# Kernel tuning notes

Hardware: AMD Instinct MI355X
Metric: run time of the kernel (lower is better)

Reference implementation:

```python
import jax, jax.numpy as jnp
import numpy as np

N = 50000       # nodes
E = 1600000     # edges
IN_C = 128
HID = 32        # hidden_channels per head
HEADS = 4
OUT_C = 64
SLOPE = 0.2     # PyG GATConv default negative_slope


def setup_inputs() -> dict:
    key = jax.random.key(0)
    ks = jax.random.split(key, 10)
    s1 = 1.0 / np.sqrt(IN_C)
    s2 = 1.0 / np.sqrt(HEADS * HID)
    return {
        "x": jax.random.normal(ks[0], (N, IN_C), dtype=jnp.float32),
        "edge_index": jax.random.randint(ks[1], (2, E), 0, N, dtype=jnp.int64),
        "W1": jax.random.normal(ks[2], (IN_C, HEADS * HID), dtype=jnp.float32) * s1,
        "a1_src": jax.random.normal(ks[3], (HEADS, HID), dtype=jnp.float32) * s2,
        "a1_dst": jax.random.normal(ks[4], (HEADS, HID), dtype=jnp.float32) * s2,
        "b1": jnp.zeros((HEADS * HID,), dtype=jnp.float32),
        "W2": jax.random.normal(ks[5], (HEADS * HID, OUT_C), dtype=jnp.float32) * s2,
        "a2_src": jax.random.normal(ks[6], (1, OUT_C), dtype=jnp.float32) * (1.0 / np.sqrt(OUT_C)),
        "a2_dst": jax.random.normal(ks[7], (1, OUT_C), dtype=jnp.float32) * (1.0 / np.sqrt(OUT_C)),
        "b2": jnp.zeros((OUT_C,), dtype=jnp.float32),
    }


def gat_conv(x, W, a_src, a_dst, b, src, dst, n, heads, out_c, concat):
    # Linear projection per head: [n, heads, out_c]
    h = (x @ W).reshape(n, heads, out_c)
    # Per-node attention halves (PyG decomposition of a^T [h_i || h_j])
    al_src = jnp.sum(h * a_src, axis=-1)  # [n, heads]
    al_dst = jnp.sum(h * a_dst, axis=-1)  # [n, heads]
    # Per-edge logits + segment softmax over destination nodes
    e = jax.nn.leaky_relu(al_src[src] + al_dst[dst], SLOPE)  # [e, heads]
    m = jax.ops.segment_max(e, dst, num_segments=n)          # [n, heads]
    ex = jnp.exp(e - m[dst])
    denom = jax.ops.segment_sum(ex, dst, num_segments=n)
    alpha = ex / denom[dst]                                   # [e, heads]
    # Weighted scatter-aggregate of source features
    out = jax.ops.segment_sum(h[src] * alpha[..., None], dst, num_segments=n)
    out = out.reshape(n, heads * out_c) if concat else out.mean(axis=1)
    return out + b


def reference(x, edge_index, W1, a1_src, a1_dst, b1, W2, a2_src, a2_dst, b2):
    # PyG GATConv adds self-loops by default
    loops = jnp.arange(N, dtype=edge_index.dtype)
    src = jnp.concatenate([edge_index[0], loops])
    dst = jnp.concatenate([edge_index[1], loops])
    h = jax.nn.elu(gat_conv(x, W1, a1_src, a1_dst, b1, src, dst, N, HEADS, HID, True))
    out = gat_conv(h, W2, a2_src, a2_dst, b2, src, dst, N, 1, OUT_C, True)
    return out
```

## Files before the change

kernel.cpp:

```cpp
#include <hip/hip_runtime.h>
#include <hip/hip_fp16.h>

#define LRELU(v) ((v) > 0.f ? (v) : 0.2f * (v))

typedef _Float16 f16;
typedef __attribute__((ext_vector_type(4))) _Float16 f16x4;
typedef __attribute__((ext_vector_type(8))) _Float16 f16x8;
typedef __attribute__((ext_vector_type(4))) float    f32x4;

__device__ __forceinline__ int swz(int row, int kbyte) {
    return (row * 256 + kbyte) ^ ((row & 7) << 4);
}

constexpr int NPB    = 128;
constexpr int MAXBUK = 512;
constexpr int EPB    = 8192;
constexpr int CAP    = 12288;

__global__ void zero_kernel(int* __restrict__ p, int n) {
    int i = blockIdx.x * blockDim.x + threadIdx.x;
    if (i < n) p[i] = 0;
}

__global__ __launch_bounds__(256) void bucket_hist_kernel(
    const int* __restrict__ ei, int* __restrict__ bcnt, int E, int tot, int nbuk) {
    __shared__ int lh[MAXBUK];
    for (int i = threadIdx.x; i < nbuk; i += 256) lh[i] = 0;
    __syncthreads();
    int base = blockIdx.x * EPB;
    int lim  = min(base + EPB, tot);
    for (int e = base + threadIdx.x; e < lim; e += 256) {
        int dst = (e < E) ? ei[E + e] : (e - E);
        atomicAdd(&lh[dst >> 7], 1);
    }
    __syncthreads();
    for (int i = threadIdx.x; i < nbuk; i += 256)
        if (lh[i]) atomicAdd(&bcnt[i], lh[i]);
}

__global__ __launch_bounds__(512) void bucket_scan_kernel(
    const int* __restrict__ bcnt, int* __restrict__ boff, int* __restrict__ bcur,
    int* __restrict__ csr_off, int nbuk, int n, int tot) {
    __shared__ int s[512];
    int t = threadIdx.x;
    int v0 = (t < nbuk) ? bcnt[t] : 0;
    s[t] = v0;
    __syncthreads();
    for (int d = 1; d < 512; d <<= 1) {
        int v = (t >= d) ? s[t - d] : 0;
        __syncthreads();
        s[t] += v;
        __syncthreads();
    }
    if (t < nbuk) {
        int off = s[t] - v0;
        boff[t] = off;
        bcur[t] = off;
    }
    if (t == 0) { boff[nbuk] = tot; csr_off[n] = tot; }
}

__global__ __launch_bounds__(256) void bucket_scatter_kernel(
    const int* __restrict__ ei, int* __restrict__ bcur, int2* __restrict__ be,
    int E, int tot, int nbuk) {
    __shared__ int lh[MAXBUK];
    __shared__ int lb[MAXBUK];
    for (int i = threadIdx.x; i < nbuk; i += 256) lh[i] = 0;
    __syncthreads();
    int base = blockIdx.x * EPB;
    int lim  = min(base + EPB, tot);
    for (int e = base + threadIdx.x; e < lim; e += 256) {
        int dst = (e < E) ? ei[E + e] : (e - E);
        atomicAdd(&lh[dst >> 7], 1);
    }
    __syncthreads();
    for (int i = threadIdx.x; i < nbuk; i += 256)
        lb[i] = lh[i] ? atomicAdd(&bcur[i], lh[i]) : 0;
    __syncthreads();
    for (int i = threadIdx.x; i < nbuk; i += 256) lh[i] = 0;
    __syncthreads();
    for (int e = base + threadIdx.x; e < lim; e += 256) {
        int src, dst;
        if (e < E) { src = ei[e]; dst = ei[E + e]; }
        else       { src = dst = e - E; }
        int b = dst >> 7;
        int p = lb[b] + atomicAdd(&lh[b], 1);
        be[p] = make_int2(src, dst);
    }
}

__global__ __launch_bounds__(256) void csr_build_kernel(
    const int2* __restrict__ be, const int* __restrict__ boff,
    int* __restrict__ csr_off, int* __restrict__ csr_src, int n) {
    __shared__ int hist[NPB];
    __shared__ int sc[NPB];
    __shared__ int cur[NPB];
    __shared__ int stage[CAP];
    const int b = blockIdx.x, t = threadIdx.x;
    const int start = boff[b], end = boff[b + 1], cnt = end - start;
    if (t < NPB) hist[t] = 0;
    __syncthreads();
    for (int i = t; i < cnt; i += 256)
        atomicAdd(&hist[be[start + i].y & (NPB - 1)], 1);
    __syncthreads();
    if (t < NPB) sc[t] = hist[t];
    __syncthreads();
    for (int d = 1; d < NPB; d <<= 1) {
        int v = (t < NPB && t >= d) ? sc[t - d] : 0;
        __syncthreads();
        if (t < NPB) sc[t] += v;
        __syncthreads();
    }
    if (t < NPB) {
        int excl = sc[t] - hist[t];
        cur[t] = excl;
        int node = b * NPB + t;
        if (node < n) csr_off[node] = start + excl;
    }
    __syncthreads();
    if (cnt <= CAP) {
        for (int i = t; i < cnt; i += 256) {
            int2 e = be[start + i];
            int  p = atomicAdd(&cur[e.y & (NPB - 1)], 1);
            stage[p] = e.x;
        }
        __syncthreads();
        for (int i = t; i < cnt; i += 256) csr_src[start + i] = stage[i];
    } else {
        for (int i = t; i < cnt; i += 256) {
            int2 e = be[start + i];
            int  p = atomicAdd(&cur[e.y & (NPB - 1)], 1);
            csr_src[start + p] = e.x;
        }
    }
}

__global__ void hist_kernel(const int* __restrict__ ei, int* __restrict__ counts,
                            int E, int tot) {
    int e = blockIdx.x * blockDim.x + threadIdx.x;
    if (e >= tot) return;
    int dst = (e < E) ? ei[E + e] : (e - E);
    atomicAdd(&counts[dst], 1);
}

__global__ __launch_bounds__(1024) void scan_kernel(const int* __restrict__ counts,
                                                    int* __restrict__ csr_off,
                                                    int* __restrict__ cursor, int n) {
    __shared__ int part[1024];
    int t = threadIdx.x;
    int chunk = (n + 1023) >> 10;
    int lo = t * chunk, hi = min(lo + chunk, n);
    int sum = 0;
    for (int i = lo; i < hi; ++i) sum += counts[i];
    part[t] = sum;
    __syncthreads();
    for (int d = 1; d < 1024; d <<= 1) {
        int add = (t >= d) ? part[t - d] : 0;
        __syncthreads();
        part[t] += add;
        __syncthreads();
    }
    int run = part[t] - sum;
    for (int i = lo; i < hi; ++i) {
        csr_off[i] = run;
        cursor[i]  = run;
        run += counts[i];
    }
    if (t == 1023) csr_off[n] = part[1023];
}

__global__ void scatter_kernel(const int* __restrict__ ei, int* __restrict__ cursor,
                               int* __restrict__ csr_src, int E, int tot) {
    int e = blockIdx.x * blockDim.x + threadIdx.x;
    if (e >= tot) return;
    int src, dst;
    if (e < E) { src = ei[e]; dst = ei[E + e]; }
    else       { src = dst = e - E; }
    int pos = atomicAdd(&cursor[dst], 1);
    csr_src[pos] = src;
}

__global__ void prep_w_kernel(const float* __restrict__ W, f16* __restrict__ WhT,
                              f16* __restrict__ WlT, int ncol) {
    int idx = blockIdx.x * 256 + threadIdx.x;
    if (idx >= 128 * ncol) return;
    int k = idx / ncol, c = idx % ncol;
    float v = W[idx];
    f16 h = (f16)v;
    f16 l = (f16)(v - (float)h);
    int byte = swz(c, k * 2);
    *(f16*)((char*)WhT + byte) = h;
    *(f16*)((char*)WlT + byte) = l;
}

template <int NCOL>
__global__ __launch_bounds__(256) void gemm_mfma_kernel(
    const float* __restrict__ x, const f16* __restrict__ WhT,
    const f16* __restrict__ WlT, __half* __restrict__ feat, int n) {
    constexpr int ROWS = 64;
    constexpr int NCT  = NCOL / 16;
    __shared__ char Xh[ROWS * 256];
    __shared__ char Xl[ROWS * 256];
    __shared__ char Wh[NCOL * 256];
    __shared__ char Wl[NCOL * 256];
    const int t  = threadIdx.x;
    const int r0 = blockIdx.x * ROWS;

    {
        const float4* sh = (const float4*)WhT;
        const float4* sl = (const float4*)WlT;
        float4* dh = (float4*)Wh;
        float4* dl = (float4*)Wl;
        for (int i = t; i < NCOL * 16; i += 256) { dh[i] = sh[i]; dl[i] = sl[i]; }
    }
    {
        const float4* X4 = (const float4*)x;
        for (int i = t; i < ROWS * 32; i += 256) {
            int row = i >> 5, k4 = i & 31;
            float4 v = (r0 + row < n) ? X4[(size_t)(r0 + row) * 32 + k4]
                                      : make_float4(0.f, 0.f, 0.f, 0.f);
            f16x4 h, l;
            h[0] = (f16)v.x; l[0] = (f16)(v.x - (float)h[0]);
            h[1] = (f16)v.y; l[1] = (f16)(v.y - (float)h[1]);
            h[2] = (f16)v.z; l[2] = (f16)(v.z - (float)h[2]);
            h[3] = (f16)v.w; l[3] = (f16)(v.w - (float)h[3]);
            int byte = swz(row, k4 * 8);
            *(f16x4*)(Xh + byte) = h;
            *(f16x4*)(Xl + byte) = l;
        }
    }
    __syncthreads();

    const int w  = t >> 6, l = t & 63;
    const int lr = l & 15, lg = l >> 4;
    const int arow = w * 16 + lr;

    f32x4 acc[NCT];
#pragma unroll
    for (int ct = 0; ct < NCT; ++ct) acc[ct] = (f32x4){0.f, 0.f, 0.f, 0.f};

#pragma unroll
    for (int kt = 0; kt < 4; ++kt) {
        const int ka = kt * 64 + 8 * lg;
        f16x4 al0 = *(const f16x4*)(Xh + swz(arow, ka));
        f16x4 al1 = *(const f16x4*)(Xh + swz(arow, ka + 32));
        f16x4 am0 = *(const f16x4*)(Xl + swz(arow, ka));
        f16x4 am1 = *(const f16x4*)(Xl + swz(arow, ka + 32));
        f16x8 a_h = __builtin_shufflevector(al0, al1, 0, 1, 2, 3, 4, 5, 6, 7);
        f16x8 a_l = __builtin_shufflevector(am0, am1, 0, 1, 2, 3, 4, 5, 6, 7);
#pragma unroll
        for (int ct = 0; ct < NCT; ++ct) {
            const int col = ct * 16 + lr;
            f16x4 b0 = *(const f16x4*)(Wh + swz(col, ka));
            f16x4 b1 = *(const f16x4*)(Wh + swz(col, ka + 32));
            f16x4 c0 = *(const f16x4*)(Wl + swz(col, ka));
            f16x4 c1 = *(const f16x4*)(Wl + swz(col, ka + 32));
            f16x8 b_h = __builtin_shufflevector(b0, b1, 0, 1, 2, 3, 4, 5, 6, 7);
            f16x8 b_l = __builtin_shufflevector(c0, c1, 0, 1, 2, 3, 4, 5, 6, 7);
            acc[ct] = __builtin_amdgcn_mfma_f32_16x16x32_f16(a_h, b_h, acc[ct], 0, 0, 0);
            acc[ct] = __builtin_amdgcn_mfma_f32_16x16x32_f16(a_l, b_h, acc[ct], 0, 0, 0);
            acc[ct] = __builtin_amdgcn_mfma_f32_16x16x32_f16(a_h, b_l, acc[ct], 0, 0, 0);
        }
    }

#pragma unroll
    for (int ct = 0; ct < NCT; ++ct)
#pragma unroll
        for (int r = 0; r < 4; ++r) {
            int grow = r0 + w * 16 + lg * 4 + r;
            if (grow < n)
                feat[(size_t)grow * NCOL + ct * 16 + lr] = __float2half(acc[ct][r]);
        }
}

template <int OUTC, int HEADS>
__global__ __launch_bounds__(256) void al_kernel(
    const __half* __restrict__ feat, const float* __restrict__ a_src,
    const float* __restrict__ a_dst, float* __restrict__ alsrc,
    float* __restrict__ aldst, int n) {
    constexpr int CP  = OUTC / 64;
    constexpr int HID = OUTC / HEADS;
    constexpr int G   = HID / CP;
    int node = blockIdx.x * 4 + (threadIdx.x >> 6);
    int lane = threadIdx.x & 63;
    if (node >= n) return;
    float s, d;
    if constexpr (CP == 2) {
        __half2 hv = *(const __half2*)(feat + (size_t)node * OUTC + lane * 2);
        float2  f  = __half22float2(hv);
        s = f.x * a_src[lane * 2] + f.y * a_src[lane * 2 + 1];
        d = f.x * a_dst[lane * 2] + f.y * a_dst[lane * 2 + 1];
    } else {
        float f = __half2float(feat[(size_t)node * OUTC + lane]);
        s = f * a_src[lane];
        d = f * a_dst[lane];
    }
#pragma unroll
    for (int o = G / 2; o > 0; o >>= 1) {
        s += __shfl_xor(s, o);
        d += __shfl_xor(d, o);
    }
    if ((lane & (G - 1)) == 0) {
        int h = lane / G;
        alsrc[node * HEADS + h] = s;
        aldst[node * HEADS + h] = d;
    }
}

template <int OUTC, int HEADS, bool DO_ELU>
__global__ __launch_bounds__(256) void aggregate_kernel(
    const int* __restrict__ csr_off, const int* __restrict__ csr_src,
    const float* __restrict__ alsrc, const float* __restrict__ aldst,
    const __half* __restrict__ feat, const float* __restrict__ bias,
    float* __restrict__ out, int n) {
    constexpr int CPL = 8;
    constexpr int LPE = OUTC / CPL;
    constexpr int EPW = 64 / LPE;
    constexpr int HID = OUTC / HEADS;
    int node = blockIdx.x * 4 + (threadIdx.x >> 6);
    int lane = threadIdx.x & 63;
    if (node >= n) return;
    int off = csr_off[node];
    int deg = csr_off[node + 1] - off;

    const int   sub = lane / LPE;
    const int   l   = lane % LPE;
    const int   h   = (CPL * l) / HID;
    const float ad  = aldst[node * HEADS + h];

    float acc[CPL];
#pragma unroll
    for (int c = 0; c < CPL; ++c) acc[c] = 0.f;
    float sume = 0.f;

#pragma unroll 2
    for (int i = sub; i < deg; i += EPW) {
        int   s = csr_src[off + i];
        float e = alsrc[(size_t)s * HEADS + h] + ad;
        e = LRELU(e);
        float p = __expf(e);
        sume += p;
        const float4   fv = *(const float4*)(feat + (size_t)s * OUTC + CPL * l);
        const __half2* hp = (const __half2*)&fv;
#pragma unroll
        for (int c2 = 0; c2 < 4; ++c2) {
            float2 f2 = __half22float2(hp[c2]);
            acc[2 * c2 + 0] += p * f2.x;
            acc[2 * c2 + 1] += p * f2.y;
        }
    }
#pragma unroll
    for (int o = LPE; o < 64; o <<= 1) {
#pragma unroll
        for (int c = 0; c < CPL; ++c) acc[c] += __shfl_xor(acc[c], o);
        sume += __shfl_xor(sume, o);
    }
    if (sub == 0) {
        const float inv = 1.f / sume;
        float v[CPL];
#pragma unroll
        for (int c = 0; c < CPL; ++c) {
            v[c] = acc[c] * inv + bias[CPL * l + c];
            if (DO_ELU) v[c] = (v[c] > 0.f) ? v[c] : expm1f(v[c]);
        }
        float* op = out + (size_t)node * OUTC + CPL * l;
        *(float4*)(op + 0) = make_float4(v[0], v[1], v[2], v[3]);
        *(float4*)(op + 4) = make_float4(v[4], v[5], v[6], v[7]);
    }
}

extern "C" void kernel_launch(void* const* d_in, const int* in_sizes, int n_in,
                              void* d_out, int out_size, void* d_ws, size_t ws_size,
                              hipStream_t stream) {
    const float* x   = (const float*)d_in[0];
    const int*   ei  = (const int*)d_in[1];
    const float* W1  = (const float*)d_in[2];
    const float* a1s = (const float*)d_in[3];
    const float* a1d = (const float*)d_in[4];
    const float* b1  = (const float*)d_in[5];
    const float* W2  = (const float*)d_in[6];
    const float* a2s = (const float*)d_in[7];
    const float* a2d = (const float*)d_in[8];
    const float* b2  = (const float*)d_in[9];
    float*       out = (float*)d_out;

    constexpr int IN_C = 128, HEADS = 4, OUTC1 = 128, OUTC2 = 64;
    const int n    = in_sizes[0] / IN_C;
    const int E    = in_sizes[1] / 2;
    const int tot  = E + n;
    const int nbuk = (n + NPB - 1) / NPB;

    char* w = (char*)d_ws;
    auto  alloc = [&](size_t bytes) -> char* {
        char* p = w;
        w += (bytes + 255) & ~(size_t)255;
        return p;
    };
    int*    bcnt    = (int*)alloc((size_t)MAXBUK * 4);
    int*    boff    = (int*)alloc((size_t)(MAXBUK + 1) * 4);
    int*    bcur    = (int*)alloc((size_t)MAXBUK * 4);
    int*    csr_off = (int*)alloc((size_t)(n + 1) * 4);
    int*    csr_src = (int*)alloc((size_t)tot * 4);
    int2*   be      = (int2*)alloc((size_t)tot * 8);
    size_t  csr_need = (size_t)(w - (char*)d_ws);
    f16*    wh1     = (f16*)alloc(128 * 256);
    f16*    wl1     = (f16*)alloc(128 * 256);
    f16*    wh2     = (f16*)alloc(64 * 256);
    f16*    wl2     = (f16*)alloc(64 * 256);
    float*  alsrc1  = (float*)alloc((size_t)n * HEADS * 4);
    float*  aldst1  = (float*)alloc((size_t)n * HEADS * 4);
    float*  alsrc2  = (float*)alloc((size_t)n * 4);
    float*  aldst2  = (float*)alloc((size_t)n * 4);
    __half* feat_h  = (__half*)alloc((size_t)n * OUTC1 * 2);
    float*  y1      = (float*)alloc((size_t)n * OUTC1 * 4);
    const bool new_csr = (nbuk <= MAXBUK) && (csr_need <= ws_size);

    prep_w_kernel<<<(128 * OUTC1 + 255) / 256, 256, 0, stream>>>(W1, wh1, wl1, OUTC1);
    prep_w_kernel<<<(128 * OUTC2 + 255) / 256, 256, 0, stream>>>(W2, wh2, wl2, OUTC2);

    if (new_csr) {
        const int g1 = (tot + EPB - 1) / EPB;
        zero_kernel<<<(nbuk + 255) / 256, 256, 0, stream>>>(bcnt, nbuk);
        bucket_hist_kernel<<<g1, 256, 0, stream>>>(ei, bcnt, E, tot, nbuk);
        bucket_scan_kernel<<<1, 512, 0, stream>>>(bcnt, boff, bcur, csr_off, nbuk, n, tot);
        bucket_scatter_kernel<<<g1, 256, 0, stream>>>(ei, bcur, be, E, tot, nbuk);
        csr_build_kernel<<<nbuk, 256, 0, stream>>>(be, boff, csr_off, csr_src, n);
    } else {
        int* counts = (int*)be;
        int* cursor = counts + n;
        zero_kernel<<<(n + 255) / 256, 256, 0, stream>>>(counts, n);
        hist_kernel<<<(tot + 255) / 256, 256, 0, stream>>>(ei, counts, E, tot);
        scan_kernel<<<1, 1024, 0, stream>>>(counts, csr_off, cursor, n);
        scatter_kernel<<<(tot + 255) / 256, 256, 0, stream>>>(ei, cursor, csr_src, E, tot);
    }

    const int gblk = (n + 63) / 64;
    gemm_mfma_kernel<OUTC1><<<gblk, 256, 0, stream>>>(x, wh1, wl1, feat_h, n);
    al_kernel<OUTC1, HEADS><<<(n + 3) / 4, 256, 0, stream>>>(
        feat_h, a1s, a1d, alsrc1, aldst1, n);
    aggregate_kernel<OUTC1, HEADS, true><<<(n + 3) / 4, 256, 0, stream>>>(
        csr_off, csr_src, alsrc1, aldst1, feat_h, b1, y1, n);

    gemm_mfma_kernel<OUTC2><<<gblk, 256, 0, stream>>>(y1, wh2, wl2, feat_h, n);
    al_kernel<OUTC2, 1><<<(n + 3) / 4, 256, 0, stream>>>(
        feat_h, a2s, a2d, alsrc2, aldst2, n);
    aggregate_kernel<OUTC2, 1, false><<<(n + 3) / 4, 256, 0, stream>>>(
        csr_off, csr_src, alsrc2, aldst2, feat_h, b2, out, n);
}
```

Measured before the change: 222.6 us.

## Fuse attention-logit computation into GEMM, pack bucket edges, batch softmax weights

```diff
diff --git a/kernel.cpp b/kernel.cpp
--- a/kernel.cpp
+++ b/kernel.cpp
@@ -14,7 +14,7 @@
 
 constexpr int NPB    = 128;
 constexpr int MAXBUK = 512;
-constexpr int EPB    = 8192;
+constexpr int EPB    = 2048;
 constexpr int CAP    = 12288;
 
 __global__ void zero_kernel(int* __restrict__ p, int n) {
@@ -61,8 +61,8 @@
 }
 
 __global__ __launch_bounds__(256) void bucket_scatter_kernel(
-    const int* __restrict__ ei, int* __restrict__ bcur, int2* __restrict__ be,
-    int E, int tot, int nbuk) {
+    const int* __restrict__ ei, int* __restrict__ bcur,
+    unsigned int* __restrict__ be, int E, int tot, int nbuk) {
     __shared__ int lh[MAXBUK];
     __shared__ int lb[MAXBUK];
     for (int i = threadIdx.x; i < nbuk; i += 256) lh[i] = 0;
@@ -85,12 +85,12 @@
         else       { src = dst = e - E; }
         int b = dst >> 7;
         int p = lb[b] + atomicAdd(&lh[b], 1);
-        be[p] = make_int2(src, dst);
+        be[p] = (unsigned)src | ((unsigned)(dst & (NPB - 1)) << 16);
     }
 }
 
 __global__ __launch_bounds__(256) void csr_build_kernel(
-    const int2* __restrict__ be, const int* __restrict__ boff,
+    const unsigned int* __restrict__ be, const int* __restrict__ boff,
     int* __restrict__ csr_off, int* __restrict__ csr_src, int n) {
     __shared__ int hist[NPB];
     __shared__ int sc[NPB];
@@ -101,7 +101,7 @@
     if (t < NPB) hist[t] = 0;
     __syncthreads();
     for (int i = t; i < cnt; i += 256)
-        atomicAdd(&hist[be[start + i].y & (NPB - 1)], 1);
+        atomicAdd(&hist[be[start + i] >> 16], 1);
     __syncthreads();
     if (t < NPB) sc[t] = hist[t];
     __syncthreads();
@@ -120,17 +120,17 @@
     __syncthreads();
     if (cnt <= CAP) {
         for (int i = t; i < cnt; i += 256) {
-            int2 e = be[start + i];
-            int  p = atomicAdd(&cur[e.y & (NPB - 1)], 1);
-            stage[p] = e.x;
+            unsigned v = be[start + i];
+            int p = atomicAdd(&cur[v >> 16], 1);
+            stage[p] = (int)(v & 0xFFFFu);
         }
         __syncthreads();
         for (int i = t; i < cnt; i += 256) csr_src[start + i] = stage[i];
     } else {
         for (int i = t; i < cnt; i += 256) {
-            int2 e = be[start + i];
-            int  p = atomicAdd(&cur[e.y & (NPB - 1)], 1);
-            csr_src[start + p] = e.x;
+            unsigned v = be[start + i];
+            int p = atomicAdd(&cur[v >> 16], 1);
+            csr_src[start + p] = (int)(v & 0xFFFFu);
         }
     }
 }
@@ -193,12 +193,15 @@
     *(f16*)((char*)WlT + byte) = l;
 }
 
-template <int NCOL>
+template <int NCOL, int HEADS>
 __global__ __launch_bounds__(256) void gemm_mfma_kernel(
     const float* __restrict__ x, const f16* __restrict__ WhT,
-    const f16* __restrict__ WlT, __half* __restrict__ feat, int n) {
+    const f16* __restrict__ WlT, const float* __restrict__ a_src,
+    const float* __restrict__ a_dst, __half* __restrict__ feat,
+    float* __restrict__ alsrc, float* __restrict__ aldst, int n) {
     constexpr int ROWS = 64;
     constexpr int NCT  = NCOL / 16;
+    constexpr int CTH  = (NCOL / HEADS) / 16;
     __shared__ char Xh[ROWS * 256];
     __shared__ char Xl[ROWS * 256];
     __shared__ char Wh[NCOL * 256];
@@ -271,39 +274,35 @@
             if (grow < n)
                 feat[(size_t)grow * NCOL + ct * 16 + lr] = __float2half(acc[ct][r]);
         }
-}
-
-template <int OUTC, int HEADS>
-__global__ __launch_bounds__(256) void al_kernel(
-    const __half* __restrict__ feat, const float* __restrict__ a_src,
-    const float* __restrict__ a_dst, float* __restrict__ alsrc,
-    float* __restrict__ aldst, int n) {
-    constexpr int CP  = OUTC / 64;
-    constexpr int HID = OUTC / HEADS;
-    constexpr int G   = HID / CP;
-    int node = blockIdx.x * 4 + (threadIdx.x >> 6);
-    int lane = threadIdx.x & 63;
-    if (node >= n) return;
-    float s, d;
-    if constexpr (CP == 2) {
-        __half2 hv = *(const __half2*)(feat + (size_t)node * OUTC + lane * 2);
-        float2  f  = __half22float2(hv);
-        s = f.x * a_src[lane * 2] + f.y * a_src[lane * 2 + 1];
-        d = f.x * a_dst[lane * 2] + f.y * a_dst[lane * 2 + 1];
-    } else {
-        float f = __half2float(feat[(size_t)node * OUTC + lane]);
-        s = f * a_src[lane];
-        d = f * a_dst[lane];
-    }
-#pragma unroll
-    for (int o = G / 2; o > 0; o >>= 1) {
-        s += __shfl_xor(s, o);
-        d += __shfl_xor(d, o);
-    }
-    if ((lane & (G - 1)) == 0) {
-        int h = lane / G;
-        alsrc[node * HEADS + h] = s;
-        aldst[node * HEADS + h] = d;
+
+    float as[NCT], av[NCT];
+#pragma unroll
+    for (int ct = 0; ct < NCT; ++ct) {
+        as[ct] = a_src[ct * 16 + lr];
+        av[ct] = a_dst[ct * 16 + lr];
+    }
+#pragma unroll
+    for (int r = 0; r < 4; ++r) {
+        int grow = r0 + w * 16 + lg * 4 + r;
+#pragma unroll
+        for (int h = 0; h < HEADS; ++h) {
+            float s = 0.f, d = 0.f;
+#pragma unroll
+            for (int q = 0; q < CTH; ++q) {
+                int ct = h * CTH + q;
+                s += acc[ct][r] * as[ct];
+                d += acc[ct][r] * av[ct];
+            }
+#pragma unroll
+            for (int o = 1; o < 16; o <<= 1) {
+                s += __shfl_xor(s, o);
+                d += __shfl_xor(d, o);
+            }
+            if (lr == 0 && grow < n) {
+                alsrc[grow * HEADS + h] = s;
+                aldst[grow * HEADS + h] = d;
+            }
+        }
     }
 }
 
@@ -317,46 +316,62 @@
     constexpr int LPE = OUTC / CPL;
     constexpr int EPW = 64 / LPE;
     constexpr int HID = OUTC / HEADS;
-    int node = blockIdx.x * 4 + (threadIdx.x >> 6);
-    int lane = threadIdx.x & 63;
+    constexpr int B   = 64 / HEADS;
+    __shared__ float pbuf[4][64];
+    const int wid  = threadIdx.x >> 6;
+    const int lane = threadIdx.x & 63;
+    int node = blockIdx.x * 4 + wid;
     if (node >= n) return;
-    int off = csr_off[node];
-    int deg = csr_off[node + 1] - off;
-
-    const int   sub = lane / LPE;
-    const int   l   = lane % LPE;
-    const int   h   = (CPL * l) / HID;
-    const float ad  = aldst[node * HEADS + h];
+    const int off = csr_off[node];
+    const int deg = csr_off[node + 1] - off;
+
+    const int   e1  = lane / HEADS;
+    const int   h1  = lane & (HEADS - 1);
+    const float ad1 = aldst[node * HEADS + h1];
+    const int sub = lane / LPE;
+    const int l   = lane % LPE;
+    const int h2  = (CPL * l) / HID;
 
     float acc[CPL];
 #pragma unroll
     for (int c = 0; c < CPL; ++c) acc[c] = 0.f;
     float sume = 0.f;
 
+    for (int base = 0; base < deg; base += B) {
+        const int bcnt = min(B, deg - base);
+        float p = 0.f;
+        if (e1 < bcnt) {
+            int   s = csr_src[off + base + e1];
+            float e = alsrc[(size_t)s * HEADS + h1] + ad1;
+            e = LRELU(e);
+            p = __expf(e);
+        }
+        pbuf[wid][lane] = p;
+        sume += p;
 #pragma unroll 2
-    for (int i = sub; i < deg; i += EPW) {
-        int   s = csr_src[off + i];
-        float e = alsrc[(size_t)s * HEADS + h] + ad;
-        e = LRELU(e);
-        float p = __expf(e);
-        sume += p;
-        const float4   fv = *(const float4*)(feat + (size_t)s * OUTC + CPL * l);
-        const __half2* hp = (const __half2*)&fv;
-#pragma unroll
-        for (int c2 = 0; c2 < 4; ++c2) {
-            float2 f2 = __half22float2(hp[c2]);
-            acc[2 * c2 + 0] += p * f2.x;
-            acc[2 * c2 + 1] += p * f2.y;
-        }
-    }
-#pragma unroll
-    for (int o = LPE; o < 64; o <<= 1) {
+        for (int i = sub; i < bcnt; i += EPW) {
+            int   s  = csr_src[off + base + i];
+            float pp = pbuf[wid][i * HEADS + h2];
+            const float4   fv = *(const float4*)(feat + (size_t)s * OUTC + CPL * l);
+            const __half2* hp = (const __half2*)&fv;
+#pragma unroll
+            for (int c2 = 0; c2 < 4; ++c2) {
+                float2 f2 = __half22float2(hp[c2]);
+                acc[2 * c2 + 0] += pp * f2.x;
+                acc[2 * c2 + 1] += pp * f2.y;
+            }
+        }
+    }
+#pragma unroll
+    for (int o = HEADS; o < 64; o <<= 1) sume += __shfl_xor(sume, o);
+    const float sume_h = __shfl(sume, h2);
+#pragma unroll
+    for (int o = LPE; o < 64; o <<= 1)
 #pragma unroll
         for (int c = 0; c < CPL; ++c) acc[c] += __shfl_xor(acc[c], o);
-        sume += __shfl_xor(sume, o);
-    }
+
     if (sub == 0) {
-        const float inv = 1.f / sume;
+        const float inv = 1.f / sume_h;
         float v[CPL];
 #pragma unroll
         for (int c = 0; c < CPL; ++c) {
@@ -401,7 +416,9 @@
     int*    bcur    = (int*)alloc((size_t)MAXBUK * 4);
     int*    csr_off = (int*)alloc((size_t)(n + 1) * 4);
     int*    csr_src = (int*)alloc((size_t)tot * 4);
-    int2*   be      = (int2*)alloc((size_t)tot * 8);
+    size_t  be_sz   = (size_t)tot * 4 > (size_t)2 * n * 4 ? (size_t)tot * 4
+                                                          : (size_t)2 * n * 4;
+    unsigned int* be = (unsigned int*)alloc(be_sz);
     size_t  csr_need = (size_t)(w - (char*)d_ws);
     f16*    wh1     = (f16*)alloc(128 * 256);
     f16*    wl1     = (f16*)alloc(128 * 256);
@@ -435,15 +452,13 @@
     }
 
     const int gblk = (n + 63) / 64;
-    gemm_mfma_kernel<OUTC1><<<gblk, 256, 0, stream>>>(x, wh1, wl1, feat_h, n);
-    al_kernel<OUTC1, HEADS><<<(n + 3) / 4, 256, 0, stream>>>(
-        feat_h, a1s, a1d, alsrc1, aldst1, n);
+    gemm_mfma_kernel<OUTC1, HEADS><<<gblk, 256, 0, stream>>>(
+        x, wh1, wl1, a1s, a1d, feat_h, alsrc1, aldst1, n);
     aggregate_kernel<OUTC1, HEADS, true><<<(n + 3) / 4, 256, 0, stream>>>(
         csr_off, csr_src, alsrc1, aldst1, feat_h, b1, y1, n);
 
-    gemm_mfma_kernel<OUTC2><<<gblk, 256, 0, stream>>>(y1, wh2, wl2, feat_h, n);
-    al_kernel<OUTC2, 1><<<(n + 3) / 4, 256, 0, stream>>>(
-        feat_h, a2s, a2d, alsrc2, aldst2, n);
+    gemm_mfma_kernel<OUTC2, 1><<<gblk, 256, 0, stream>>>(
+        y1, wh2, wl2, a2s, a2d, feat_h, alsrc2, aldst2, n);
     aggregate_kernel<OUTC2, 1, false><<<(n + 3) / 4, 256, 0, stream>>>(
         csr_off, csr_src, alsrc2, aldst2, feat_h, b2, out, n);
 }
```

New measurement: 247.5 us. 1.11x slower.
